# Performance work log

Hardware: AMD Instinct MI355X
Metric: run time of the kernel (lower is better)

Reference implementation:

```python
import jax, jax.numpy as jnp
import numpy as np

B, T, D, HD = 4, 4096, 1024, 64

def setup_inputs() -> dict:
    key = jax.random.key(0)
    k1, k2, k3, k4 = jax.random.split(key, 4)
    scale = 1.0 / np.sqrt(D)
    return {
        "x": jax.random.normal(k1, (B, T, D), dtype=jnp.float32),
        "Wq": jax.random.normal(k2, (HD, D), dtype=jnp.float32) * scale,
        "Wk": jax.random.normal(k3, (HD, D), dtype=jnp.float32) * scale,
        "Wv": jax.random.normal(k4, (HD, D), dtype=jnp.float32) * scale,
    }

def reference(x, Wq, Wk, Wv):
    # x: [B,T,D]; W*: [head_dim, D] (torch Linear weight layout)
    Q = jnp.einsum('btd,hd->bth', x, Wq)  # [B,T,HD]
    K = jnp.einsum('btd,hd->bth', x, Wk)
    V = jnp.einsum('btd,hd->bth', x, Wv)
    hd = Q.shape[-1]
    scores = jnp.einsum('bqh,bkh->bqk', Q, K) * (hd ** -0.5)  # [B,T,T]
    t = scores.shape[1]
    causal = jnp.tril(jnp.ones((t, t), dtype=bool))
    scores = jnp.where(causal, scores, -jnp.inf)
    att = jax.nn.softmax(scores, axis=-1)
    return jnp.einsum('bqk,bkh->bqh', att, V)  # [B,T,HD]
```

## Files before the change

kernel.cpp:

```cpp
#include <hip/hip_runtime.h>
#include <stdint.h>

#define B_  4
#define T_  4096
#define D_  1024
#define HD_ 64
#define BT_ 16384

typedef short bf16x8 __attribute__((ext_vector_type(8)));
typedef float f32x4  __attribute__((ext_vector_type(4)));
typedef float f32x16 __attribute__((ext_vector_type(16)));
typedef unsigned short u16;
typedef u16 u16x4 __attribute__((ext_vector_type(4)));
typedef unsigned int u32;
typedef u32 u32x4 __attribute__((ext_vector_type(4)));

#define M0L2_  11.54156032f
#define QSCALE_ 0.18033688f

#define CPB_   264
#define NSLOT_ (4 * CPB_ * 2)

__device__ __forceinline__ u16 f2bf(float f) {
    union { float f; unsigned u; } v; v.f = f;
    unsigned r = (v.u + 0x7FFF + ((v.u >> 16) & 1)) >> 16;
    return (u16)r;
}
__device__ __forceinline__ float bf2f(u16 u) {
    union { unsigned u; float f; } v; v.u = ((unsigned)u) << 16;
    return v.f;
}
__device__ __forceinline__ u32 cvt_pk_bf16(float lo, float hi) {
    u32 r;
    asm("v_cvt_pk_bf16_f32 %0, %1, %2" : "=v"(r) : "v"(lo), "v"(hi));
    return r;
}

__global__ __launch_bounds__(256) void wconv_kernel(
    const float* __restrict__ wq, const float* __restrict__ wk,
    const float* __restrict__ wv, u16* __restrict__ wb)
{
    const int j   = blockIdx.x >> 5;
    const int off = (blockIdx.x & 31) * 2048 + threadIdx.x * 8;
    const float* src = (j == 0) ? wq : ((j == 1) ? wk : wv);
    f32x4 a0 = *(const f32x4*)(src + off);
    f32x4 a1 = *(const f32x4*)(src + off + 4);
    u32x4 b;
    b[0] = cvt_pk_bf16(a0[0], a0[1]);
    b[1] = cvt_pk_bf16(a0[2], a0[3]);
    b[2] = cvt_pk_bf16(a1[0], a1[1]);
    b[3] = cvt_pk_bf16(a1[2], a1[3]);
    *(u32x4*)(wb + j * 65536 + off) = b;
}

__global__ __launch_bounds__(512) void qkv_kernel(
    const float* __restrict__ x, const u16* __restrict__ wb,
    u16* __restrict__ qs, u16* __restrict__ kss, u16* __restrict__ vssT)
{
    __shared__ __align__(16) u16 xt[64][72];
    __shared__ __align__(16) u16 wt[192][72];

    const int tid  = threadIdx.x;
    const int lane = tid & 63;
    const int w    = tid >> 6;
    const int quad = lane >> 4;
    const int l16  = lane & 15;
    const int row0 = blockIdx.x * 64;
    const int rh   = w >> 2;
    const int ct   = w & 3;

    const int xrow = tid >> 3;
    const int xcg  = tid & 7;

    f32x4 acc[2][3];
    #pragma unroll
    for (int s = 0; s < 2; ++s)
        #pragma unroll
        for (int g = 0; g < 3; ++g) acc[s][g] = (f32x4)0.0f;

    f32x4 xa, xb;
    bf16x8 wr[3];
    {
        const float* xp = x + (size_t)(row0 + xrow) * D_ + xcg * 8;
        xa = *(const f32x4*)xp; xb = *(const f32x4*)(xp + 4);
        #pragma unroll
        for (int i = 0; i < 3; ++i) {
            int chunk = tid + 512 * i;
            wr[i] = *(const bf16x8*)(wb + (size_t)(chunk >> 3) * D_ + (chunk & 7) * 8);
        }
    }

    for (int kc = 0; kc < 16; ++kc) {
        __syncthreads();
        {
            u32x4 px;
            px[0] = cvt_pk_bf16(xa[0], xa[1]);
            px[1] = cvt_pk_bf16(xa[2], xa[3]);
            px[2] = cvt_pk_bf16(xb[0], xb[1]);
            px[3] = cvt_pk_bf16(xb[2], xb[3]);
            *(u32x4*)&xt[xrow][xcg * 8] = px;
            #pragma unroll
            for (int i = 0; i < 3; ++i) {
                int chunk = tid + 512 * i;
                *(bf16x8*)&wt[chunk >> 3][(chunk & 7) * 8] = wr[i];
            }
        }
        __syncthreads();
        if (kc < 15) {
            const float* xp = x + (size_t)(row0 + xrow) * D_ + (kc + 1) * 64 + xcg * 8;
            xa = *(const f32x4*)xp; xb = *(const f32x4*)(xp + 4);
            #pragma unroll
            for (int i = 0; i < 3; ++i) {
                int chunk = tid + 512 * i;
                wr[i] = *(const bf16x8*)(wb + (size_t)(chunk >> 3) * D_ + (kc + 1) * 64 + (chunk & 7) * 8);
            }
        }
        #pragma unroll
        for (int ks = 0; ks < 2; ++ks) {
            bf16x8 a[2];
            #pragma unroll
            for (int s = 0; s < 2; ++s)
                a[s] = *(const bf16x8*)&xt[rh * 32 + s * 16 + l16][ks * 32 + quad * 8];
            #pragma unroll
            for (int g = 0; g < 3; ++g) {
                bf16x8 bfr = *(const bf16x8*)&wt[(ct * 3 + g) * 16 + l16][ks * 32 + quad * 8];
                #pragma unroll
                for (int s = 0; s < 2; ++s)
                    acc[s][g] = __builtin_amdgcn_mfma_f32_16x16x32_bf16(a[s], bfr, acc[s][g], 0, 0, 0);
            }
        }
    }
    #pragma unroll
    for (int s = 0; s < 2; ++s) {
        #pragma unroll
        for (int g = 0; g < 3; ++g) {
            const int n = (ct * 3 + g) * 16 + l16;
            const int j = n >> 6, h = n & 63;
            const int rbase = row0 + rh * 32 + s * 16 + quad * 4;
            if (j == 0) {
                #pragma unroll
                for (int r = 0; r < 4; ++r) qs[(size_t)(rbase + r) * HD_ + h] = f2bf(acc[s][g][r] * QSCALE_);
            } else if (j == 1) {
                #pragma unroll
                for (int r = 0; r < 4; ++r) kss[(size_t)(rbase + r) * HD_ + h] = f2bf(acc[s][g][r]);
            } else {
                u16x4 v;
                #pragma unroll
                for (int r = 0; r < 4; ++r) v[r] = f2bf(acc[s][g][r]);
                *(u16x4*)(vssT + (size_t)h * BT_ + rbase) = v;
            }
        }
    }
}

__global__ __launch_bounds__(256, 4) void attn_kernel(
    const u16* __restrict__ qs, const u16* __restrict__ kss,
    const u16* __restrict__ vssT,
    float* __restrict__ pl, u16* __restrict__ pO)
{
    __shared__ __align__(16) u16 kt2[8 * 65 * 8];
    __shared__ __align__(16) u16 vt2[8 * 65 * 8];

    const int m = blockIdx.x % CPB_;
    const int b = blockIdx.x / CPB_;

    int t0, bound, qtA, qtB;
    if (m < 240)      { int u = m >> 4; t0 = (m & 15) * 4; bound = 2 * u + 2; qtA = u;  qtB = 30 - u; }
    else if (m < 248) { t0 = (m - 240) * 4; bound = 1 << 30; qtA = 15; qtB = 15; }
    else              { t0 = (m - 248) * 4; bound = 1 << 30; qtA = 31; qtB = 31; }

    const int tid  = threadIdx.x;
    const int lane = tid & 63;
    const int w    = tid >> 6;
    const int l31  = lane & 31;
    const int hi   = lane >> 5;
    const size_t base = (size_t)b * T_;

    int qt    = (t0 < bound) ? qtA : qtB;
    int kti   = (t0 < bound) ? t0 : (t0 - bound);
    int qrow0 = qt * 128 + w * 32;

    bf16x8 qf[4];
    #pragma unroll
    for (int ds = 0; ds < 4; ++ds)
        qf[ds] = *(const bf16x8*)(qs + (base + qrow0 + l31) * HD_ + ds * 16 + hi * 8);

    f32x16 o0 = (f32x16)0.0f, o1 = (f32x16)0.0f;
    float l_acc = 0.0f;

    const int srow = tid >> 2, q4 = tid & 3;
    const u16* kp = kss  + (base + srow) * HD_ + q4 * 16;
    const u16* vp = vssT + (size_t)srow * BT_ + base + q4 * 16;
    u16* kdst = kt2 + ((((srow >> 5) * 4 + q4) * 65 + (srow & 31)) * 8);
    u16* vdst = vt2 + ((((srow >> 5) * 4 + q4) * 65 + (srow & 31)) * 8);

    bf16x8 kr0, kr1, vr0, vr1;
    {
        const u16* k0 = kp + (size_t)kti * 64 * HD_;
        kr0 = *(const bf16x8*)k0; kr1 = *(const bf16x8*)(k0 + 8);
        const u16* v0 = vp + kti * 64;
        vr0 = *(const bf16x8*)v0; vr1 = *(const bf16x8*)(v0 + 8);
    }

    auto FLUSH = [&](int role) {
        const int slot = (b * CPB_ + m) * 2 + role;
        u32 la = __builtin_bit_cast(u32, l_acc), lb = la;
        asm("v_permlane32_swap_b32 %0, %1" : "+v"(la), "+v"(lb));
        float lfull = __builtin_bit_cast(float, la) + __builtin_bit_cast(float, lb);
        if (hi == 0) pl[slot * 128 + w * 32 + l31] = lfull;
        #pragma unroll
        for (int reg = 0; reg < 16; ++reg) {
            int row = w * 32 + (reg & 3) + 8 * (reg >> 2) + 4 * hi;
            pO[(size_t)slot * 8192 + row * 64 + l31]      = f2bf(o0[reg]);
            pO[(size_t)slot * 8192 + row * 64 + 32 + l31] = f2bf(o1[reg]);
        }
    };

    for (int step = 0; step < 4; ++step) {
        const int i = t0 + step;
        __syncthreads();
        *(bf16x8*)(kdst)       = kr0;
        *(bf16x8*)(kdst + 256) = kr1;
        *(bf16x8*)(vdst)       = vr0;
        *(bf16x8*)(vdst + 256) = vr1;
        __syncthreads();

        int kti_next = 0;
        if (step < 3) {
            kti_next = (i + 1 < bound) ? (i + 1) : (i + 1 - bound);
            const u16* k0 = kp + (size_t)kti_next * 64 * HD_;
            kr0 = *(const bf16x8*)k0; kr1 = *(const bf16x8*)(k0 + 8);
            const u16* v0 = vp + kti_next * 64;
            vr0 = *(const bf16x8*)v0; vr1 = *(const bf16x8*)(v0 + 8);
        }

        if (kti * 64 <= qrow0 + 31) {
            const bool diag = (kti * 64 + 63 > qrow0);
            const int  qa   = qrow0 + l31;
            u32 wv[16];
            #pragma unroll
            for (int kg = 0; kg < 2; ++kg) {
                f32x16 s = (f32x16)0.0f;
                __builtin_amdgcn_s_setprio(1);
                #pragma unroll
                for (int ds = 0; ds < 4; ++ds) {
                    bf16x8 af = *(const bf16x8*)(kt2 + ((kg * 4 + ds) * 65 + lane) * 8);
                    s = __builtin_amdgcn_mfma_f32_32x32x16_bf16(af, qf[ds], s, 0, 0, 0);
                }
                __builtin_amdgcn_s_setprio(0);
                float lp = 0.0f;
                #pragma unroll
                for (int rp = 0; rp < 8; ++rp) {
                    float e0 = __builtin_amdgcn_exp2f(s[2 * rp]     - M0L2_);
                    float e1 = __builtin_amdgcn_exp2f(s[2 * rp + 1] - M0L2_);
                    if (diag) {
                        const int k0e = kti * 64 + kg * 32 + ((2 * rp) & 3) + 8 * ((2 * rp) >> 2) + 4 * hi;
                        if (k0e > qa)     e0 = 0.0f;
                        if (k0e + 1 > qa) e1 = 0.0f;
                    }
                    lp += e0 + e1;
                    wv[kg * 8 + rp] = cvt_pk_bf16(e0, e1);
                }
                l_acc += lp;
            }
            bf16x8 pa[4];
            #pragma unroll
            for (int ks = 0; ks < 4; ++ks) {
                const int kg2 = ks >> 1, k1 = ks & 1;
                u32 x0 = wv[kg2 * 8 + k1 * 4 + 0], y0 = wv[kg2 * 8 + k1 * 4 + 2];
                u32 x1 = wv[kg2 * 8 + k1 * 4 + 1], y1 = wv[kg2 * 8 + k1 * 4 + 3];
                asm("v_permlane32_swap_b32 %0, %1" : "+v"(x0), "+v"(y0));
                asm("v_permlane32_swap_b32 %0, %1" : "+v"(x1), "+v"(y1));
                u32x4 t; t[0] = x0; t[1] = x1; t[2] = y0; t[3] = y1;
                pa[ks] = __builtin_bit_cast(bf16x8, t);
            }
            __builtin_amdgcn_s_setprio(1);
            #pragma unroll
            for (int ks = 0; ks < 4; ++ks) {
                bf16x8 vf0 = *(const bf16x8*)(vt2 + ((0 * 4 + ks) * 65 + lane) * 8);
                o0 = __builtin_amdgcn_mfma_f32_32x32x16_bf16(pa[ks], vf0, o0, 0, 0, 0);
                bf16x8 vf1 = *(const bf16x8*)(vt2 + ((1 * 4 + ks) * 65 + lane) * 8);
                o1 = __builtin_amdgcn_mfma_f32_32x32x16_bf16(pa[ks], vf1, o1, 0, 0, 0);
            }
            __builtin_amdgcn_s_setprio(0);
        }

        kti = kti_next;
        if (step < 3 && (i + 1) == bound) {
            FLUSH(0);
            o0 = (f32x16)0.0f; o1 = (f32x16)0.0f; l_acc = 0.0f;
            qt = qtB; qrow0 = qt * 128 + w * 32;
            #pragma unroll
            for (int ds = 0; ds < 4; ++ds)
                qf[ds] = *(const bf16x8*)(qs + (base + qrow0 + l31) * HD_ + ds * 16 + hi * 8);
        }
    }
    FLUSH((t0 + 3 >= bound) ? 1 : 0);
}

__global__ __launch_bounds__(256) void merge_kernel(
    const float* __restrict__ pl, const u16* __restrict__ pO,
    float* __restrict__ out)
{
    const int bi  = blockIdx.x;
    const int rh  = bi & 1;
    const int qt2 = (bi >> 1) & 31;
    const int b   = bi >> 6;

    int c0, c1, role, mbase;
    if (qt2 <= 14)      { int u = qt2;      c0 = 0;                 c1 = (2 * u + 1) >> 2; role = 0; mbase = u * 16; }
    else if (qt2 == 15) { c0 = 0;           c1 = 7;                 role = 0; mbase = 240; }
    else if (qt2 <= 30) { int u = 30 - qt2; c0 = (2 * u + 2) >> 2;  c1 = 15; role = 1; mbase = u * 16; }
    else                { c0 = 0;           c1 = 15;                role = 0; mbase = 248; }

    const int row = rh * 64 + (threadIdx.x >> 2);
    const int hg  = (threadIdx.x & 3) * 16;

    float L = 0.0f;
    float o[16];
    #pragma unroll
    for (int i = 0; i < 16; ++i) o[i] = 0.0f;
    for (int c = c0; c <= c1; ++c) {
        const int slot = (b * CPB_ + mbase + c) * 2 + role;
        L += pl[slot * 128 + row];
        const u16* p = pO + (size_t)slot * 8192 + row * 64 + hg;
        bf16x8 v0 = *(const bf16x8*)p;
        bf16x8 v1 = *(const bf16x8*)(p + 8);
        #pragma unroll
        for (int i = 0; i < 8; ++i) { o[i] += bf2f((u16)v0[i]); o[8 + i] += bf2f((u16)v1[i]); }
    }
    const float inv = 1.0f / L;
    float* op = out + ((size_t)b * T_ + qt2 * 128 + row) * HD_ + hg;
    #pragma unroll
    for (int j = 0; j < 4; ++j) {
        f32x4 v;
        #pragma unroll
        for (int i = 0; i < 4; ++i) v[i] = o[j * 4 + i] * inv;
        *(f32x4*)(op + j * 4) = v;
    }
}

extern "C" void kernel_launch(void* const* d_in, const int* in_sizes, int n_in,
                              void* d_out, int out_size, void* d_ws, size_t ws_size,
                              hipStream_t stream) {
    const float* x  = (const float*)d_in[0];
    const float* wq = (const float*)d_in[1];
    const float* wk = (const float*)d_in[2];
    const float* wv = (const float*)d_in[3];

    const size_t NE = (size_t)BT_ * HD_;
    char* ws = (char*)d_ws;
    u16* qs   = (u16*)ws;
    u16* kss  = qs  + NE;
    u16* vssT = kss + NE;
    u16* wb   = vssT + NE;
    float* pl = (float*)(wb + 192 * 1024);
    u16* pO   = (u16*)(pl + (size_t)NSLOT_ * 128);
    float* out = (float*)d_out;

    wconv_kernel<<<dim3(96),        dim3(256), 0, stream>>>(wq, wk, wv, wb);
    qkv_kernel  <<<dim3(256),       dim3(512), 0, stream>>>(x, wb, qs, kss, vssT);
    attn_kernel <<<dim3(4 * CPB_),  dim3(256), 0, stream>>>(qs, kss, vssT, pl, pO);
    merge_kernel<<<dim3(256),       dim3(256), 0, stream>>>(pl, pO, out);
}
```

Measured before the change: 150.9 us.

## Double-buffer LDS tiles and prefetch two K-chunks ahead in QKV projection

The QKV projection kernel now uses two LDS buffers for the x and weight tiles and keeps two register stage sets, so global loads run two chunks ahead. Each chunk needs one barrier instead of two. This is meant to hide global-load latency behind the MFMA work. In exchange it doubles LDS use (about 55KB per block), raises register pressure, and adds a launch-bounds occupancy hint. The QKV stage is only part of the total time, next to the attention kernel.

After: 146.3 us. -3.1%, faster.

```diff
diff --git a/kernel.cpp b/kernel.cpp
--- a/kernel.cpp
+++ b/kernel.cpp
@@ -53,12 +53,14 @@
     *(u32x4*)(wb + j * 65536 + off) = b;
 }
 
-__global__ __launch_bounds__(512) void qkv_kernel(
+struct StageSet { f32x4 xa, xb; bf16x8 w0, w1, w2; };
+
+__global__ __launch_bounds__(512, 2) void qkv_kernel(
     const float* __restrict__ x, const u16* __restrict__ wb,
     u16* __restrict__ qs, u16* __restrict__ kss, u16* __restrict__ vssT)
 {
-    __shared__ __align__(16) u16 xt[64][72];
-    __shared__ __align__(16) u16 wt[192][72];
+    __shared__ __align__(16) u16 xt[2][64][72];
+    __shared__ __align__(16) u16 wt[2][192][72];
 
     const int tid  = threadIdx.x;
     const int lane = tid & 63;
@@ -78,58 +80,64 @@
         #pragma unroll
         for (int g = 0; g < 3; ++g) acc[s][g] = (f32x4)0.0f;
 
-    f32x4 xa, xb;
-    bf16x8 wr[3];
-    {
-        const float* xp = x + (size_t)(row0 + xrow) * D_ + xcg * 8;
-        xa = *(const f32x4*)xp; xb = *(const f32x4*)(xp + 4);
-        #pragma unroll
-        for (int i = 0; i < 3; ++i) {
-            int chunk = tid + 512 * i;
-            wr[i] = *(const bf16x8*)(wb + (size_t)(chunk >> 3) * D_ + (chunk & 7) * 8);
-        }
-    }
-
-    for (int kc = 0; kc < 16; ++kc) {
-        __syncthreads();
-        {
-            u32x4 px;
-            px[0] = cvt_pk_bf16(xa[0], xa[1]);
-            px[1] = cvt_pk_bf16(xa[2], xa[3]);
-            px[2] = cvt_pk_bf16(xb[0], xb[1]);
-            px[3] = cvt_pk_bf16(xb[2], xb[3]);
-            *(u32x4*)&xt[xrow][xcg * 8] = px;
-            #pragma unroll
-            for (int i = 0; i < 3; ++i) {
-                int chunk = tid + 512 * i;
-                *(bf16x8*)&wt[chunk >> 3][(chunk & 7) * 8] = wr[i];
-            }
-        }
-        __syncthreads();
-        if (kc < 15) {
-            const float* xp = x + (size_t)(row0 + xrow) * D_ + (kc + 1) * 64 + xcg * 8;
-            xa = *(const f32x4*)xp; xb = *(const f32x4*)(xp + 4);
-            #pragma unroll
-            for (int i = 0; i < 3; ++i) {
-                int chunk = tid + 512 * i;
-                wr[i] = *(const bf16x8*)(wb + (size_t)(chunk >> 3) * D_ + (kc + 1) * 64 + (chunk & 7) * 8);
-            }
-        }
+    const float* xbase = x + (size_t)(row0 + xrow) * D_ + xcg * 8;
+    const int    wrow  = tid >> 3;
+
+    auto load_tile = [&](StageSet& S, int t) {
+        const float* xp = xbase + t * 64;
+        S.xa = *(const f32x4*)xp; S.xb = *(const f32x4*)(xp + 4);
+        const u16* wp = wb + t * 64;
+        S.w0 = *(const bf16x8*)(wp + (size_t)((tid       ) >> 3) * D_ + ((tid       ) & 7) * 8);
+        S.w1 = *(const bf16x8*)(wp + (size_t)((tid +  512) >> 3) * D_ + ((tid +  512) & 7) * 8);
+        S.w2 = *(const bf16x8*)(wp + (size_t)((tid + 1024) >> 3) * D_ + ((tid + 1024) & 7) * 8);
+    };
+    auto store_tile = [&](const StageSet& S, int bufi) {
+        u32x4 px;
+        px[0] = cvt_pk_bf16(S.xa[0], S.xa[1]);
+        px[1] = cvt_pk_bf16(S.xa[2], S.xa[3]);
+        px[2] = cvt_pk_bf16(S.xb[0], S.xb[1]);
+        px[3] = cvt_pk_bf16(S.xb[2], S.xb[3]);
+        *(u32x4*)&xt[bufi][xrow][xcg * 8] = px;
+        *(bf16x8*)&wt[bufi][(tid       ) >> 3][((tid       ) & 7) * 8] = S.w0;
+        *(bf16x8*)&wt[bufi][(tid +  512) >> 3][((tid +  512) & 7) * 8] = S.w1;
+        *(bf16x8*)&wt[bufi][(tid + 1024) >> 3][((tid + 1024) & 7) * 8] = S.w2;
+    };
+    auto compute = [&](int bufi) {
         #pragma unroll
         for (int ks = 0; ks < 2; ++ks) {
             bf16x8 a[2];
             #pragma unroll
             for (int s = 0; s < 2; ++s)
-                a[s] = *(const bf16x8*)&xt[rh * 32 + s * 16 + l16][ks * 32 + quad * 8];
+                a[s] = *(const bf16x8*)&xt[bufi][rh * 32 + s * 16 + l16][ks * 32 + quad * 8];
             #pragma unroll
             for (int g = 0; g < 3; ++g) {
-                bf16x8 bfr = *(const bf16x8*)&wt[(ct * 3 + g) * 16 + l16][ks * 32 + quad * 8];
+                bf16x8 bfr = *(const bf16x8*)&wt[bufi][(ct * 3 + g) * 16 + l16][ks * 32 + quad * 8];
                 #pragma unroll
                 for (int s = 0; s < 2; ++s)
                     acc[s][g] = __builtin_amdgcn_mfma_f32_16x16x32_bf16(a[s], bfr, acc[s][g], 0, 0, 0);
             }
         }
-    }
+    };
+
+    StageSet A, B;
+    load_tile(A, 0);
+    load_tile(B, 1);
+    store_tile(A, 0);
+    __syncthreads();
+
+    #pragma unroll
+    for (int kc2 = 0; kc2 < 8; ++kc2) {
+        const int kc = kc2 * 2;
+        if (kc + 2 < 16) load_tile(A, kc + 2);
+        compute(0);
+        store_tile(B, 1);
+        __syncthreads();
+        if (kc + 3 < 16) load_tile(B, kc + 3);
+        compute(1);
+        if (kc + 2 < 16) store_tile(A, 0);
+        __syncthreads();
+    }
+
     #pragma unroll
     for (int s = 0; s < 2; ++s) {
         #pragma unroll
```
